# Performance work log

Hardware: AMD Instinct MI355X
Metric: run time of the kernel (lower is better)

Reference implementation:

```python
import jax, jax.numpy as jnp
import numpy as np

N_ENTITY = 100000
H_DIM = 512
N_ROWS = 262144
ALPHA = 0.5          # EMA rate for fast state
GATE_TH = 0.5        # gate_threshold buffer
GATE_SCALE = 5.0     # gate_scale buffer
LN_EPS = 1e-5


def setup_inputs() -> dict:
    key = jax.random.key(0)
    k1, k2, k3, k4, k5 = jax.random.split(key, 5)
    entity_emb = jax.random.normal(k1, (N_ROWS, H_DIM), dtype=jnp.float32)
    entity_ids = jax.random.randint(k2, (N_ROWS,), 0, N_ENTITY, dtype=jnp.int64)
    slow_state = 0.1 * jax.random.normal(k3, (N_ENTITY, H_DIM), dtype=jnp.float32)
    fast_state = 0.1 * jax.random.normal(k4, (N_ENTITY, H_DIM), dtype=jnp.float32)
    # torch nn.Linear(2h, h): weight shape (h, 2h), y = x @ W.T + b
    W = jax.random.normal(k5, (H_DIM, 2 * H_DIM), dtype=jnp.float32) * 0.02
    b = jnp.zeros((H_DIM,), dtype=jnp.float32)
    return {"entity_emb": entity_emb, "slow_state": slow_state,
            "fast_state": fast_state, "W": W, "b": b, "entity_ids": entity_ids}


def _layer_norm(x):
    mu = jnp.mean(x, axis=-1, keepdims=True)
    var = jnp.mean(jnp.square(x - mu), axis=-1, keepdims=True)
    return (x - mu) * jax.lax.rsqrt(var + LN_EPS)


def reference(entity_emb, slow_state, fast_state, W, b, entity_ids):
    # ---- fuse_with_state (gate path) ----
    state = slow_state[entity_ids]                                   # (N, h) gather
    is_active = (jnp.sum(jnp.abs(state), axis=-1, keepdims=True) > 1e-6).astype(entity_emb.dtype)
    h_state = _layer_norm(state)
    gate_in = jnp.concatenate([entity_emb, h_state], axis=-1)        # (N, 2h)
    z = jax.nn.sigmoid(gate_in @ W.T + b)                            # (N, h)
    fused = z * entity_emb + (1.0 - z) * h_state
    out = is_active * fused + (1.0 - is_active) * entity_emb

    # ---- writeback (no-grad in torch; scatter-reduce EMA + norm-gated slow update) ----
    ctx = jax.lax.stop_gradient(out)
    ids = entity_ids
    counts = jax.ops.segment_sum(jnp.ones((ctx.shape[0],), ctx.dtype), ids,
                                 num_segments=N_ENTITY)              # (E,)
    ctx_sum = jax.ops.segment_sum(ctx, ids, num_segments=N_ENTITY)   # (E, h)
    ctx_mean = ctx_sum / jnp.clip(counts, 1.0)[:, None]
    touched = (counts > 0)[:, None]
    new_fast_all = (1.0 - ALPHA) * fast_state + ALPHA * ctx_mean
    new_fast = jnp.where(touched, new_fast_all, fast_state)
    diff = new_fast - slow_state
    delta = jnp.linalg.norm(diff, axis=-1, keepdims=True)
    gate = jax.nn.sigmoid(GATE_SCALE * (delta - GATE_TH))
    new_slow = jnp.where(touched, slow_state + gate * diff, slow_state)
    return out, new_fast, new_slow
```

## Files before the change

### kernel.cpp

```cpp
#include <hip/hip_runtime.h>
#include <hip/hip_bf16.h>
#include <cstdint>

#define NROWS 262144
#define HDIM  512
#define NENT  100000
#define SCAN_NBLK ((NENT + 1023) / 1024)

typedef __attribute__((ext_vector_type(4))) float  f32x4;
typedef __attribute__((ext_vector_type(8))) short  bf16x8;
typedef __attribute__((ext_vector_type(4))) short  bf16x4;

static __device__ __forceinline__ unsigned short f2bf(float x) {
    unsigned u = __float_as_uint(x);
    u += 0x7FFF + ((u >> 16) & 1);
    return (unsigned short)(u >> 16);
}

__global__ void pack_w_kernel(const float* __restrict__ W, unsigned short* __restrict__ Wp) {
    int g    = blockIdx.x * 256 + threadIdx.x;
    int lane = g & 63;
    int nt   = (g >> 6) & 31;
    int kt   = g >> 11;
    int col  = nt * 16 + (lane & 15);
    int k    = kt * 32 + ((lane >> 4) << 3);
    const float* src = W + (size_t)col * 1024 + k;
    f32x4 v0 = *(const f32x4*)(src);
    f32x4 v1 = *(const f32x4*)(src + 4);
    bf16x8 ov;
#pragma unroll
    for (int i = 0; i < 4; ++i) {
        ov[i]     = (short)f2bf(v0[i]);
        ov[4 + i] = (short)f2bf(v1[i]);
    }
    *(bf16x8*)(Wp + (size_t)g * 8) = ov;
}

__global__ __launch_bounds__(256) void count_kernel(const int* __restrict__ ids,
                                                    unsigned* __restrict__ counts) {
    int r = blockIdx.x * 256 + threadIdx.x;
    if (r < NROWS) atomicAdd(&counts[ids[r]], 1u);
}

__global__ __launch_bounds__(1024) void scan1_kernel(const unsigned* __restrict__ counts,
                                                     unsigned* __restrict__ off,
                                                     unsigned* __restrict__ bsums) {
    __shared__ unsigned tmp[1024];
    int i = blockIdx.x * 1024 + threadIdx.x;
    unsigned v = (i < NENT) ? counts[i] : 0u;
    tmp[threadIdx.x] = v;
    __syncthreads();
#pragma unroll
    for (int o = 1; o < 1024; o <<= 1) {
        unsigned a = (threadIdx.x >= o) ? tmp[threadIdx.x - o] : 0u;
        __syncthreads();
        tmp[threadIdx.x] += a;
        __syncthreads();
    }
    if (i < NENT) off[i] = tmp[threadIdx.x] - v;
    if (threadIdx.x == 1023) bsums[blockIdx.x] = tmp[1023];
}

__global__ void scan2_kernel(unsigned* __restrict__ bsums) {
    if (threadIdx.x == 0 && blockIdx.x == 0) {
        unsigned s = 0;
        for (int i = 0; i < SCAN_NBLK; ++i) { unsigned t = bsums[i]; bsums[i] = s; s += t; }
    }
}

__global__ __launch_bounds__(1024) void scan3_kernel(unsigned* __restrict__ off,
                                                     const unsigned* __restrict__ bsums,
                                                     unsigned* __restrict__ cursor) {
    int i = blockIdx.x * 1024 + threadIdx.x;
    if (i < NENT) {
        unsigned o = off[i] + bsums[blockIdx.x];
        off[i] = o;
        cursor[i] = o;
    }
    if (i == 0) off[NENT] = NROWS;
}

__global__ __launch_bounds__(256) void fill_kernel(const int* __restrict__ ids,
                                                   unsigned* __restrict__ cursor,
                                                   int* __restrict__ rowidx) {
    int r = blockIdx.x * 256 + threadIdx.x;
    if (r < NROWS) {
        unsigned p = atomicAdd(&cursor[ids[r]], 1u);
        rowidx[p] = r;
    }
}

__global__ __launch_bounds__(1024, 4) void fuse_kernel(
    const float* __restrict__ emb, const float* __restrict__ slow,
    const unsigned short* __restrict__ Wp, const float* __restrict__ bias,
    const int* __restrict__ ids, float* __restrict__ out)
{
    __shared__ unsigned short wLds[2][2048 * 8];
    __shared__ unsigned short xLds[2][512 * 8];
    __shared__ float muS[128], rsS[128], actS[128], bS[512];
    __shared__ int idS[128];

    const int t    = threadIdx.x;
    const int w    = t >> 6;
    const int lane = t & 63;
    const int wm   = w >> 3;
    const int wn   = w & 7;
    const int brow = blockIdx.x * 128;

    if (t < 128) ((f32x4*)bS)[t] = ((const f32x4*)bias)[t];

    for (int rr = 0; rr < 8; ++rr) {
        int row = w * 8 + rr;
        int id  = ids[brow + row];
        const float* sp = slow + (size_t)id * HDIM;
        f32x4 v0 = ((const f32x4*)sp)[lane * 2];
        f32x4 v1 = ((const f32x4*)sp)[lane * 2 + 1];
        float s = 0.f, s2 = 0.f, sa = 0.f;
#pragma unroll
        for (int i = 0; i < 4; ++i) {
            s  += v0[i] + v1[i];
            s2 += v0[i] * v0[i] + v1[i] * v1[i];
            sa += fabsf(v0[i]) + fabsf(v1[i]);
        }
#pragma unroll
        for (int m = 32; m >= 1; m >>= 1) {
            s  += __shfl_xor(s, m);
            s2 += __shfl_xor(s2, m);
            sa += __shfl_xor(sa, m);
        }
        if (lane == 0) {
            float mu  = s * (1.f / HDIM);
            float var = s2 * (1.f / HDIM) - mu * mu;
            muS[row]  = mu;
            rsS[row]  = rsqrtf(var + 1e-5f);
            actS[row] = (sa > 1e-6f) ? 1.f : 0.f;
            idS[row]  = id;
        }
    }
    __syncthreads();

    const int xrow = t >> 3;
    const int kloc = (t & 7) * 4;
    const float* srcState = slow + (size_t)idS[xrow] * HDIM + kloc;
    const float* srcEmb   = emb + (size_t)(brow + xrow) * HDIM + kloc;
    const float muR = muS[xrow], rsR = rsS[xrow];
    const int xByte = (((xrow >> 4) * 64 + (((kloc >> 3) << 4) | (xrow & 15))) << 4) + ((kloc & 7) << 1);

    f32x4 zero4 = {0.f, 0.f, 0.f, 0.f};
    f32x4 acc[4][4];
#pragma unroll
    for (int i = 0; i < 4; ++i)
#pragma unroll
        for (int j = 0; j < 4; ++j) acc[i][j] = zero4;

#define ISSUE(ph, wr0, wr1, xr)                                          \
    {   int ktW = ((ph) < 16) ? (16 + (ph)) : ((ph) - 16);               \
        const bf16x8* wp = (const bf16x8*)(Wp + (size_t)ktW * 16384);    \
        wr0 = wp[t];                                                     \
        wr1 = wp[t + 1024];                                              \
        const float* xp = ((ph) < 16) ? (srcState + (ph) * 32)           \
                                      : (srcEmb + ((ph) - 16) * 32);     \
        xr = *(const f32x4*)xp;                                          \
    }

#define COMMIT(ph, buf, wr0, wr1, xr)                                    \
    {   ((bf16x8*)wLds[buf])[t]        = wr0;                            \
        ((bf16x8*)wLds[buf])[t + 1024] = wr1;                            \
        f32x4 y = xr;                                                    \
        if ((ph) < 16) {                                                 \
            _Pragma("unroll")                                            \
            for (int i = 0; i < 4; ++i) y[i] = (y[i] - muR) * rsR;       \
        }                                                                \
        bf16x4 xv;                                                       \
        _Pragma("unroll")                                                \
        for (int i = 0; i < 4; ++i) xv[i] = (short)f2bf(y[i]);           \
        *(bf16x4*)((char*)xLds[buf] + xByte) = xv;                       \
    }

    {   bf16x8 wr0, wr1; f32x4 xr;
        ISSUE(0, wr0, wr1, xr);
        COMMIT(0, 0, wr0, wr1, xr);
    }
    __syncthreads();

    for (int ph = 0; ph < 32; ++ph) {
        const int cur = ph & 1;
        bf16x8 wr0, wr1; f32x4 xr;
        if (ph < 31) ISSUE(ph + 1, wr0, wr1, xr);

        bf16x8 wf0 = ((const bf16x8*)wLds[cur])[(wn * 4 + 0) * 64 + lane];
        bf16x8 wf1 = ((const bf16x8*)wLds[cur])[(wn * 4 + 1) * 64 + lane];
        bf16x8 wf2 = ((const bf16x8*)wLds[cur])[(wn * 4 + 2) * 64 + lane];
        bf16x8 wf3 = ((const bf16x8*)wLds[cur])[(wn * 4 + 3) * 64 + lane];
#pragma unroll
        for (int rt = 0; rt < 4; ++rt) {
            bf16x8 xf = ((const bf16x8*)xLds[cur])[(wm * 4 + rt) * 64 + lane];
            acc[rt][0] = __builtin_amdgcn_mfma_f32_16x16x32_bf16(wf0, xf, acc[rt][0], 0, 0, 0);
            acc[rt][1] = __builtin_amdgcn_mfma_f32_16x16x32_bf16(wf1, xf, acc[rt][1], 0, 0, 0);
            acc[rt][2] = __builtin_amdgcn_mfma_f32_16x16x32_bf16(wf2, xf, acc[rt][2], 0, 0, 0);
            acc[rt][3] = __builtin_amdgcn_mfma_f32_16x16x32_bf16(wf3, xf, acc[rt][3], 0, 0, 0);
        }

        if (ph < 31) COMMIT(ph + 1, cur ^ 1, wr0, wr1, xr);
        __syncthreads();
    }
#undef ISSUE
#undef COMMIT

#pragma unroll
    for (int rt = 0; rt < 4; ++rt) {
        int rowl = wm * 64 + rt * 16 + (lane & 15);
        int grow = brow + rowl;
        int id   = idS[rowl];
        float mu = muS[rowl], rs = rsS[rowl], act = actS[rowl];
        const float* embP  = emb  + (size_t)grow * HDIM;
        const float* slowP = slow + (size_t)id * HDIM;
        float*       outP  = out  + (size_t)grow * HDIM;
#pragma unroll
        for (int ct = 0; ct < 4; ++ct) {
            int col0 = wn * 64 + ct * 16 + ((lane >> 4) << 2);
            f32x4 bv = *(const f32x4*)&bS[col0];
            f32x4 ev = *(const f32x4*)(embP + col0);
            f32x4 sv = *(const f32x4*)(slowP + col0);
            f32x4 o;
#pragma unroll
            for (int r = 0; r < 4; ++r) {
                float logit = acc[rt][ct][r] + bv[r];
                float z  = 1.f / (1.f + __expf(-logit));
                float h  = (sv[r] - mu) * rs;
                float fused = z * ev[r] + (1.f - z) * h;
                o[r] = (act > 0.f) ? fused : ev[r];
            }
            *(f32x4*)(outP + col0) = o;
        }
    }
}

__global__ __launch_bounds__(256) void finalize_kernel(
    const float* __restrict__ fast, const float* __restrict__ slow,
    const float* __restrict__ out, const unsigned* __restrict__ off,
    const int* __restrict__ rowidx, float* __restrict__ nf, float* __restrict__ ns)
{
    int e = blockIdx.x * 4 + (threadIdx.x >> 6);
    if (e >= NENT) return;
    int lane = threadIdx.x & 63;
    size_t base = (size_t)e * HDIM + lane * 8;

    f32x4 f0 = *(const f32x4*)(fast + base), f1 = *(const f32x4*)(fast + base + 4);
    f32x4 l0 = *(const f32x4*)(slow + base), l1 = *(const f32x4*)(slow + base + 4);

    unsigned o0 = off[e], o1 = off[e + 1];
    int c = (int)(o1 - o0);

    if (c == 0) {
        *(f32x4*)(nf + base)     = f0;
        *(f32x4*)(nf + base + 4) = f1;
        *(f32x4*)(ns + base)     = l0;
        *(f32x4*)(ns + base + 4) = l1;
        return;
    }

    f32x4 s0 = {0.f, 0.f, 0.f, 0.f}, s1 = {0.f, 0.f, 0.f, 0.f};
    for (int j = 0; j < c; ++j) {
        int r = rowidx[o0 + j];
        const float* p = out + (size_t)r * HDIM + lane * 8;
        s0 += *(const f32x4*)p;
        s1 += *(const f32x4*)(p + 4);
    }

    float inv = 0.5f / (float)c;
    f32x4 n0, n1, d0, d1;
    float ss = 0.f;
#pragma unroll
    for (int i = 0; i < 4; ++i) {
        n0[i] = 0.5f * f0[i] + s0[i] * inv;
        n1[i] = 0.5f * f1[i] + s1[i] * inv;
        d0[i] = n0[i] - l0[i]; ss += d0[i] * d0[i];
        d1[i] = n1[i] - l1[i]; ss += d1[i] * d1[i];
    }
#pragma unroll
    for (int m = 32; m >= 1; m >>= 1) ss += __shfl_xor(ss, m);
    float delta = sqrtf(ss);
    float gate  = 1.f / (1.f + expf(-5.f * (delta - 0.5f)));

    f32x4 o0v, o1v;
#pragma unroll
    for (int i = 0; i < 4; ++i) {
        o0v[i] = l0[i] + gate * d0[i];
        o1v[i] = l1[i] + gate * d1[i];
    }
    *(f32x4*)(nf + base)     = n0;
    *(f32x4*)(nf + base + 4) = n1;
    *(f32x4*)(ns + base)     = o0v;
    *(f32x4*)(ns + base + 4) = o1v;
}

extern "C" void kernel_launch(void* const* d_in, const int* in_sizes, int n_in,
                              void* d_out, int out_size, void* d_ws, size_t ws_size,
                              hipStream_t stream) {
    const float* emb  = (const float*)d_in[0];
    const float* slow = (const float*)d_in[1];
    const float* fast = (const float*)d_in[2];
    const float* W    = (const float*)d_in[3];
    const float* bias = (const float*)d_in[4];
    const int*   ids  = (const int*)d_in[5];

    float* out = (float*)d_out;
    float* nf  = out + (size_t)NROWS * HDIM;
    float* ns  = nf + (size_t)NENT * HDIM;

    unsigned short* Wp   = (unsigned short*)d_ws;
    unsigned* counts     = (unsigned*)((char*)d_ws + (1u << 20));
    unsigned* off        = (unsigned*)((char*)d_ws + (1u << 20) + 512 * 1024);
    unsigned* bsums      = (unsigned*)((char*)d_ws + (2u << 20));
    int*      rowidx     = (int*)((char*)d_ws + (2u << 20) + 4096);

    hipMemsetAsync(counts, 0, (size_t)NENT * sizeof(unsigned), stream);

    pack_w_kernel<<<256, 256, 0, stream>>>(W, Wp);
    count_kernel<<<NROWS / 256, 256, 0, stream>>>(ids, counts);
    scan1_kernel<<<SCAN_NBLK, 1024, 0, stream>>>(counts, off, bsums);
    scan2_kernel<<<1, 64, 0, stream>>>(bsums);
    scan3_kernel<<<SCAN_NBLK, 1024, 0, stream>>>(off, bsums, counts);
    fill_kernel<<<NROWS / 256, 256, 0, stream>>>(ids, counts, rowidx);
    fuse_kernel<<<NROWS / 128, 1024, 0, stream>>>(emb, slow, Wp, bias, ids, out);
    finalize_kernel<<<(NENT + 3) / 4, 256, 0, stream>>>(fast, slow, out, off, rowidx, nf, ns);
}
```

Baseline: 1.032 ms.

## Halve fuse block tile and stream weights into LDS with global_load_lds

```diff
diff --git a/kernel.cpp b/kernel.cpp
--- a/kernel.cpp
+++ b/kernel.cpp
@@ -15,6 +15,12 @@
     unsigned u = __float_as_uint(x);
     u += 0x7FFF + ((u >> 16) & 1);
     return (unsigned short)(u >> 16);
+}
+
+static __device__ __forceinline__ void gll16(const void* g, void* l) {
+    __builtin_amdgcn_global_load_lds(
+        (const __attribute__((address_space(1))) unsigned int*)g,
+        (__attribute__((address_space(3))) unsigned int*)l, 16, 0, 0);
 }
 
 __global__ void pack_w_kernel(const float* __restrict__ W, unsigned short* __restrict__ Wp) {
@@ -90,22 +96,20 @@
     }
 }
 
-__global__ __launch_bounds__(1024, 4) void fuse_kernel(
+__global__ __launch_bounds__(512, 4) void fuse_kernel(
     const float* __restrict__ emb, const float* __restrict__ slow,
     const unsigned short* __restrict__ Wp, const float* __restrict__ bias,
     const int* __restrict__ ids, float* __restrict__ out)
 {
-    __shared__ unsigned short wLds[2][2048 * 8];
-    __shared__ unsigned short xLds[2][512 * 8];
-    __shared__ float muS[128], rsS[128], actS[128], bS[512];
-    __shared__ int idS[128];
+    __shared__ unsigned short wT[2048 * 8];
+    __shared__ unsigned short xT[2][256 * 8];
+    __shared__ float muS[64], rsS[64], actS[64], bS[512];
+    __shared__ int idS[64];
 
     const int t    = threadIdx.x;
     const int w    = t >> 6;
     const int lane = t & 63;
-    const int wm   = w >> 3;
-    const int wn   = w & 7;
-    const int brow = blockIdx.x * 128;
+    const int brow = blockIdx.x * 64;
 
     if (t < 128) ((f32x4*)bS)[t] = ((const f32x4*)bias)[t];
 
@@ -140,11 +144,11 @@
     __syncthreads();
 
     const int xrow = t >> 3;
-    const int kloc = (t & 7) * 4;
-    const float* srcState = slow + (size_t)idS[xrow] * HDIM + kloc;
-    const float* srcEmb   = emb + (size_t)(brow + xrow) * HDIM + kloc;
+    const int k4   = (t & 7) * 4;
+    const float* srcSt = slow + (size_t)idS[xrow] * HDIM + k4;
+    const float* srcEm = emb + (size_t)(brow + xrow) * HDIM + k4;
     const float muR = muS[xrow], rsR = rsS[xrow];
-    const int xByte = (((xrow >> 4) * 64 + (((kloc >> 3) << 4) | (xrow & 15))) << 4) + ((kloc & 7) << 1);
+    const int xByte = (((xrow >> 4) * 64 + (((k4 >> 3) << 4) | (xrow & 15))) << 4) + ((k4 & 7) << 1);
 
     f32x4 zero4 = {0.f, 0.f, 0.f, 0.f};
     f32x4 acc[4][4];
@@ -153,63 +157,60 @@
 #pragma unroll
         for (int j = 0; j < 4; ++j) acc[i][j] = zero4;
 
-#define ISSUE(ph, wr0, wr1, xr)                                          \
-    {   int ktW = ((ph) < 16) ? (16 + (ph)) : ((ph) - 16);               \
-        const bf16x8* wp = (const bf16x8*)(Wp + (size_t)ktW * 16384);    \
-        wr0 = wp[t];                                                     \
-        wr1 = wp[t + 1024];                                              \
-        const float* xp = ((ph) < 16) ? (srcState + (ph) * 32)           \
-                                      : (srcEmb + ((ph) - 16) * 32);     \
-        xr = *(const f32x4*)xp;                                          \
-    }
-
-#define COMMIT(ph, buf, wr0, wr1, xr)                                    \
-    {   ((bf16x8*)wLds[buf])[t]        = wr0;                            \
-        ((bf16x8*)wLds[buf])[t + 1024] = wr1;                            \
-        f32x4 y = xr;                                                    \
-        if ((ph) < 16) {                                                 \
-            _Pragma("unroll")                                            \
-            for (int i = 0; i < 4; ++i) y[i] = (y[i] - muR) * rsR;       \
-        }                                                                \
-        bf16x4 xv;                                                       \
-        _Pragma("unroll")                                                \
-        for (int i = 0; i < 4; ++i) xv[i] = (short)f2bf(y[i]);           \
-        *(bf16x4*)((char*)xLds[buf] + xByte) = xv;                       \
-    }
-
-    {   bf16x8 wr0, wr1; f32x4 xr;
-        ISSUE(0, wr0, wr1, xr);
-        COMMIT(0, 0, wr0, wr1, xr);
-    }
-    __syncthreads();
+#define LOAD_X(ph, xr)                                                   \
+    {   const float* p = ((ph) < 16) ? (srcSt + (ph) * 32)               \
+                                     : (srcEm + ((ph) - 16) * 32);       \
+        xr = *(const f32x4*)p;                                           \
+    }
+
+    f32x4 xr;
+    LOAD_X(0, xr);
 
     for (int ph = 0; ph < 32; ++ph) {
         const int cur = ph & 1;
-        bf16x8 wr0, wr1; f32x4 xr;
-        if (ph < 31) ISSUE(ph + 1, wr0, wr1, xr);
-
-        bf16x8 wf0 = ((const bf16x8*)wLds[cur])[(wn * 4 + 0) * 64 + lane];
-        bf16x8 wf1 = ((const bf16x8*)wLds[cur])[(wn * 4 + 1) * 64 + lane];
-        bf16x8 wf2 = ((const bf16x8*)wLds[cur])[(wn * 4 + 2) * 64 + lane];
-        bf16x8 wf3 = ((const bf16x8*)wLds[cur])[(wn * 4 + 3) * 64 + lane];
+        if (ph) __syncthreads();
+
+        {
+            f32x4 y = xr;
+            if (ph < 16) {
+#pragma unroll
+                for (int i = 0; i < 4; ++i) y[i] = (y[i] - muR) * rsR;
+            }
+            bf16x4 xv;
+#pragma unroll
+            for (int i = 0; i < 4; ++i) xv[i] = (short)f2bf(y[i]);
+            *(bf16x4*)((char*)xT[cur] + xByte) = xv;
+        }
+        {
+            const int ktW = (ph < 16) ? (16 + ph) : (ph - 16);
+            const unsigned short* wsrc = Wp + (size_t)ktW * 16384;
+#pragma unroll
+            for (int i = 0; i < 4; ++i)
+                gll16(wsrc + (size_t)(i * 512 + t) * 8,
+                      (char*)wT + i * 8192 + w * 1024 + lane * 16);
+        }
+        __syncthreads();
+
+        if (ph < 31) LOAD_X(ph + 1, xr);
+
+        bf16x8 wf0 = *(const bf16x8*)((char*)wT + ((w * 4 + 0) * 64 + lane) * 16);
+        bf16x8 wf1 = *(const bf16x8*)((char*)wT + ((w * 4 + 1) * 64 + lane) * 16);
+        bf16x8 wf2 = *(const bf16x8*)((char*)wT + ((w * 4 + 2) * 64 + lane) * 16);
+        bf16x8 wf3 = *(const bf16x8*)((char*)wT + ((w * 4 + 3) * 64 + lane) * 16);
 #pragma unroll
         for (int rt = 0; rt < 4; ++rt) {
-            bf16x8 xf = ((const bf16x8*)xLds[cur])[(wm * 4 + rt) * 64 + lane];
+            bf16x8 xf = *(const bf16x8*)((char*)xT[cur] + ((rt * 64 + lane) * 16));
             acc[rt][0] = __builtin_amdgcn_mfma_f32_16x16x32_bf16(wf0, xf, acc[rt][0], 0, 0, 0);
             acc[rt][1] = __builtin_amdgcn_mfma_f32_16x16x32_bf16(wf1, xf, acc[rt][1], 0, 0, 0);
             acc[rt][2] = __builtin_amdgcn_mfma_f32_16x16x32_bf16(wf2, xf, acc[rt][2], 0, 0, 0);
             acc[rt][3] = __builtin_amdgcn_mfma_f32_16x16x32_bf16(wf3, xf, acc[rt][3], 0, 0, 0);
         }
-
-        if (ph < 31) COMMIT(ph + 1, cur ^ 1, wr0, wr1, xr);
-        __syncthreads();
-    }
-#undef ISSUE
-#undef COMMIT
+    }
+#undef LOAD_X
 
 #pragma unroll
     for (int rt = 0; rt < 4; ++rt) {
-        int rowl = wm * 64 + rt * 16 + (lane & 15);
+        int rowl = rt * 16 + (lane & 15);
         int grow = brow + rowl;
         int id   = idS[rowl];
         float mu = muS[rowl], rs = rsS[rowl], act = actS[rowl];
@@ -218,7 +219,7 @@
         float*       outP  = out  + (size_t)grow * HDIM;
 #pragma unroll
         for (int ct = 0; ct < 4; ++ct) {
-            int col0 = wn * 64 + ct * 16 + ((lane >> 4) << 2);
+            int col0 = w * 64 + ct * 16 + ((lane >> 4) << 2);
             f32x4 bv = *(const f32x4*)&bS[col0];
             f32x4 ev = *(const f32x4*)(embP + col0);
             f32x4 sv = *(const f32x4*)(slowP + col0);
@@ -323,6 +324,6 @@
     scan2_kernel<<<1, 64, 0, stream>>>(bsums);
     scan3_kernel<<<SCAN_NBLK, 1024, 0, stream>>>(off, bsums, counts);
     fill_kernel<<<NROWS / 256, 256, 0, stream>>>(ids, counts, rowidx);
-    fuse_kernel<<<NROWS / 128, 1024, 0, stream>>>(emb, slow, Wp, bias, ids, out);
+    fuse_kernel<<<NROWS / 64, 512, 0, stream>>>(emb, slow, Wp, bias, ids, out);
     finalize_kernel<<<(NENT + 3) / 4, 256, 0, stream>>>(fast, slow, out, off, rowidx, nf, ns);
 }
```

Measured after the change: 1.029 ms. Within noise of the previous version (-0.3%).
